# Optimization experiments

Measured on AMD Instinct MI355X. Metric: run time of the kernel, lower is better.

Reference implementation:

```python
import jax, jax.numpy as jnp
import numpy as np
import math

B, S, SIG, EMB, LAT, H, L_ENC, L_DEC = 16, 1024, 256, 256, 256, 8, 2, 2
EH, DH = EMB // H, LAT // H
EPS = 1e-10


def _sinusoidal_last_row(d):
    # last row of a standard sinusoidal PE table (position index = max_len-1)
    pos = 5000.0 - 1.0
    i = np.arange(d)
    angles = pos / np.power(10000.0, (2 * (i // 2)) / d)
    pe = np.where(i % 2 == 0, np.sin(angles), np.cos(angles))
    return jnp.asarray(pe, dtype=jnp.float32)


def setup_inputs() -> dict:
    key = jax.random.key(0)
    ks = iter(jax.random.split(key, 64))
    w = lambda *sh: 0.05 * jax.random.normal(next(ks), sh, dtype=jnp.float32)
    z = lambda *sh: jnp.zeros(sh, dtype=jnp.float32)
    d = {
        'inputData': jax.random.normal(next(ks), (B, S, SIG), dtype=jnp.float32),
        'pos_enc': _sinusoidal_last_row(SIG),
        'embW': w(SIG, EMB), 'embb': z(EMB),
        'qW': w(EMB, EMB), 'qb': z(EMB),
        'kW': w(EMB, EMB), 'kb': z(EMB),
        'vW': w(EMB, EMB), 'vb': z(EMB),
        'encBW': w(EH, EH), 'encBb': z(EH),
        'oW': w(EMB, EMB), 'ob': z(EMB),
        'ffe_W1': w(EMB, 2 * EMB), 'ffe_b1': z(2 * EMB),
        'ffe_W2': w(2 * EMB, EMB), 'ffe_b2': z(EMB),
        'lnSA_g': jnp.ones((L_ENC, EMB)), 'lnSA_b': z(L_ENC, EMB),
        'lnFF_g': jnp.ones((L_ENC, EMB)), 'lnFF_b': z(L_ENC, EMB),
        'start': w(1, LAT),
        'decQW': w(LAT, LAT), 'decQb': z(LAT),
        'decKW': w(EMB, EMB), 'decKb': z(EMB),
        'decVW': w(EMB, LAT), 'decVb': z(LAT),
        'decBW': w(EH + DH, DH), 'decBb': z(DH),
        'latW': w(LAT, LAT), 'latb': z(LAT),
        'ffd_W1': w(LAT, LAT // 2), 'ffd_b1': z(LAT // 2),
        'ffd_W2': w(LAT // 2, LAT), 'ffd_b2': z(LAT),
        'lnCA_g': jnp.ones((L_DEC, LAT)), 'lnCA_b': z(L_DEC, LAT),
        'lnLFF_g': jnp.ones((L_DEC, LAT)), 'lnLFF_b': z(L_DEC, LAT),
        'finW': w(LAT, LAT), 'finb': z(LAT),
    }
    return d


def _ln(x, g, b):
    m = x.mean(-1, keepdims=True)
    v = x.var(-1, keepdims=True)
    return (x - m) * jax.lax.rsqrt(v + EPS) * g + b


def _enc_attn(x, qW, qb, kW, kb, vW, vb, bW, bb, oW, ob):
    # x: (B,S,EMB) -> heads (B,H,S,EH)
    sp = lambda t: t.reshape(B, S, H, EH).transpose(0, 2, 1, 3)
    q, k, v = sp(x @ qW + qb), sp(x @ kW + kb), sp(x @ vW + vb)
    bk = k @ bW + bb                                   # bilinear key (B,H,S,EH)
    attn = jax.nn.softmax(jnp.einsum('bhqd,bhkd->bhqk', q, bk) / math.sqrt(EH), axis=-1)
    out = jnp.einsum('bhqk,bhkd->bhqd', attn, v)
    out = out.transpose(0, 2, 1, 3).reshape(B, S, EMB)
    return out @ oW + ob


def _dec_attn(enc, lat, qW, qb, kW, kb, vW, vb, bW, bb, oW, ob):
    # lat: (B,LAT) single query token; enc: (B,S,EMB)
    q = (lat @ qW + qb).reshape(B, 1, H, DH).transpose(0, 2, 1, 3)   # (B,H,1,DH)
    k = (enc @ kW + kb).reshape(B, S, H, EH).transpose(0, 2, 1, 3)   # (B,H,S,EH)
    v = (enc @ vW + vb).reshape(B, S, H, DH).transpose(0, 2, 1, 3)   # (B,H,S,DH)
    qcat = jnp.broadcast_to(q, (B, H, S, DH))
    kcat = jnp.concatenate([k, qcat], axis=-1)                       # (B,H,S,EH+DH)
    bk = kcat @ bW + bb                                              # (B,H,S,DH)
    attn = jax.nn.softmax(jnp.einsum('bhqd,bhkd->bhqk', q, bk) / math.sqrt(EH + DH), axis=-1)
    out = jnp.einsum('bhqk,bhkd->bhqd', attn, v)                     # (B,H,1,DH)
    out = out.transpose(0, 2, 1, 3).reshape(B, LAT)
    return out @ oW + ob


def reference(inputData, pos_enc, embW, embb, qW, qb, kW, kb, vW, vb, encBW, encBb,
              oW, ob, ffe_W1, ffe_b1, ffe_W2, ffe_b2, lnSA_g, lnSA_b, lnFF_g, lnFF_b,
              start, decQW, decQb, decKW, decKb, decVW, decVb, decBW, decBb,
              latW, latb, ffd_W1, ffd_b1, ffd_W2, ffd_b2, lnCA_g, lnCA_b,
              lnLFF_g, lnLFF_b, finW, finb):
    emb = (inputData + pos_enc) @ embW + embb          # (B,S,EMB)
    t = emb
    for l in range(L_ENC):
        n = _ln(t, lnSA_g[l], lnSA_b[l])
        a = _enc_attn(n, qW, qb, kW, kb, vW, vb, encBW, encBb, oW, ob) + n
        t = a + emb
        n2 = _ln(t, lnFF_g[l], lnFF_b[l])
        ff = jax.nn.selu(n2 @ ffe_W1 + ffe_b1) @ ffe_W2 + ffe_b2
        t = ff + n2
    init_lat = jnp.broadcast_to(start, (B, LAT))
    lat = init_lat
    for l in range(L_DEC):
        nl = _ln(init_lat, lnCA_g[l], lnCA_b[l])       # module always feeds initialLatentData
        lat = _dec_attn(t, nl, decQW, decQb, decKW, decKb, decVW, decVb,
                        decBW, decBb, latW, latb)
        nf = _ln(lat, lnLFF_g[l], lnLFF_b[l])
        lat = jax.nn.selu(nf @ ffd_W1 + ffd_b1) @ ffd_W2 + ffd_b2
    return lat @ finW + finb
```

## Files before the change

### kernel.cpp

```cpp
#include <hip/hip_runtime.h>
#include <hip/hip_bf16.h>
#include <math.h>

typedef __hip_bfloat16 bf16;

#define BB 16
#define SS 1024
#define NH 8
#define NR (BB*SS)
#define SZE ((size_t)NR*256)
#define RS 264
#define HS 520

typedef __attribute__((ext_vector_type(8))) short short8;
typedef __attribute__((ext_vector_type(4))) float f32x4;
typedef __attribute__((ext_vector_type(8))) unsigned short u16x8;
typedef __attribute__((ext_vector_type(4))) unsigned short u16x4;

__device__ __forceinline__ float bf2f(bf16 x){ return __bfloat162float(x); }
__device__ __forceinline__ bf16  f2bf(float x){ return __float2bfloat16(x); }
__device__ __forceinline__ unsigned short f2bfu(float x){
  bf16 t = __float2bfloat16(x); return *reinterpret_cast<unsigned short*>(&t);
}
__device__ __forceinline__ float bfu2f(unsigned short u){
  return __uint_as_float(((unsigned)u)<<16);
}

__device__ __forceinline__ float ldT(const float* p, size_t i){ return p[i]; }
__device__ __forceinline__ float ldT(const bf16*  p, size_t i){ return bf2f(p[i]); }
__device__ __forceinline__ void  stT(float* p, size_t i, float v){ p[i] = v; }
__device__ __forceinline__ void  stT(bf16*  p, size_t i, float v){ p[i] = f2bf(v); }

__device__ __forceinline__ float selu_f(float x){
  const float a = 1.6732632423543772f, sc = 1.0507009873554805f;
  return sc * (x > 0.f ? x : a * expm1f(x));
}

struct PtrPack { const void* p[43]; };
struct TabPack { int off[43]; int cnt[43]; int total; };
struct TrTab   { int srcOff[12]; int K[12]; int N[12]; int dstOff[12]; int total; };

__global__ __launch_bounds__(256) void k_canon(PtrPack ptrs, TabPack tab,
    float* __restrict__ dst, int* __restrict__ flagw)
{
  unsigned w0 = ((const unsigned*)ptrs.p[18])[0];
  int isbf = (w0 == 0x3F803F80u) ? 1 : 0;
  if (blockIdx.x == 0 && threadIdx.x == 0) *flagw = isbf;
  __shared__ int so[43], sn[43];
  int tid = threadIdx.x;
  if (tid < 43){ so[tid] = tab.off[tid]; sn[tid] = tab.cnt[tid]; }
  __syncthreads();
  int g = blockIdx.x*256 + tid;
  if (g >= tab.total) return;
  int seg = 1;
  while (seg < 42 && g >= so[seg] + sn[seg]) seg++;
  int li = g - so[seg];
  float v = isbf ? bf2f(((const bf16*)ptrs.p[seg])[li])
                 : ((const float*)ptrs.p[seg])[li];
  dst[g] = v;
}

__global__ __launch_bounds__(256) void k_transW(const float* __restrict__ wt,
    TrTab tt, unsigned short* __restrict__ dst)
{
  int g = blockIdx.x*256 + threadIdx.x;
  if (g >= tt.total) return;
  int seg = 0;
  while (seg < 11 && g >= tt.dstOff[seg] + tt.K[seg]*tt.N[seg]) seg++;
  int li = g - tt.dstOff[seg];
  int K = tt.K[seg], N = tt.N[seg];
  int n = li / K, k = li - n*K;
  dst[g] = f2bfu(wt[tt.srcOff[seg] + (size_t)k*N + n]);
}

template<int K, int LDA>
__device__ __forceinline__ void wave_gemm64(const unsigned short (*As)[LDA],
    const unsigned short* __restrict__ Wt, int n0, f32x4 acc[4][4], int lane)
{
  int col = lane & 15, quad = lane >> 4;
  #pragma unroll
  for (int k0 = 0; k0 < K; k0 += 32){
    short8 a[4], b[4];
    #pragma unroll
    for (int rt = 0; rt < 4; rt++)
      a[rt] = *(const short8*)(&As[rt*16 + col][k0 + quad*8]);
    #pragma unroll
    for (int ct = 0; ct < 4; ct++)
      b[ct] = *(const short8*)(&Wt[(size_t)(n0 + ct*16 + col)*K + k0 + quad*8]);
    #pragma unroll
    for (int rt = 0; rt < 4; rt++)
      #pragma unroll
      for (int ct = 0; ct < 4; ct++)
        acc[rt][ct] = __builtin_amdgcn_mfma_f32_16x16x32_bf16(a[rt], b[ct], acc[rt][ct], 0, 0, 0);
  }
}

#define ZERO_ACC(acc) { _Pragma("unroll") for (int rt=0;rt<4;rt++){ _Pragma("unroll") for (int ct=0;ct<4;ct++) acc[rt][ct] = (f32x4){0.f,0.f,0.f,0.f}; } }

#define EPI_BEGIN(e) { int rt = (e)>>4, ct = ((e)>>2)&3, r = (e)&3; \
    int lrow = rt*16 + quad*4 + r; int gcol0 = ct*16 + col; \
    float av = acc[rt][ct][r]; (void)lrow; (void)gcol0; (void)av;
#define EPI_END }

template<int PRE, typename OT>
__global__ __launch_bounds__(256) void k_gemm_mfma(const void* __restrict__ A,
    const int* __restrict__ flagp, const float* __restrict__ pe,
    const unsigned short* __restrict__ Wt, const float* __restrict__ bias,
    OT* __restrict__ out)
{
  __shared__ __align__(16) unsigned short As[64][RS];
  int tid = threadIdx.x, row0 = blockIdx.x*64;
  if (PRE == 0){
    int f = *flagp;
    for (int jj = 0; jj < 64; jj++){
      int idx = tid + jj*256, row = idx>>8, c = idx&255;
      size_t g = (size_t)(row0+row)*256 + c;
      float x = f ? bf2f(((const bf16*)A)[g]) : ((const float*)A)[g];
      As[row][c] = f2bfu(x + pe[c]);
    }
  } else {
    for (int jj = 0; jj < 64; jj++){
      int idx = tid + jj*256, row = idx>>8, c = idx&255;
      As[row][c] = f2bfu(((const float*)A)[(size_t)(row0+row)*256 + c]);
    }
  }
  __syncthreads();
  int w = tid>>6, lane = tid&63, col = lane&15, quad = lane>>4;
  f32x4 acc[4][4];
  ZERO_ACC(acc);
  wave_gemm64<256, RS>(As, Wt, w*64, acc, lane);
  #pragma unroll
  for (int e = 0; e < 64; e++){
    EPI_BEGIN(e)
    int grow = row0 + lrow, gcol = w*64 + gcol0;
    stT(out, (size_t)grow*256 + gcol, av + bias[gcol]);
    EPI_END
  }
}

__global__ __launch_bounds__(256) void k_qkvbk_mfma(const float* __restrict__ tsrc,
    const float* __restrict__ lng, const float* __restrict__ lnb,
    const unsigned short* __restrict__ qWt, const float* __restrict__ qb,
    const unsigned short* __restrict__ kWt, const float* __restrict__ kb,
    const unsigned short* __restrict__ vWt, const float* __restrict__ vb,
    const unsigned short* __restrict__ encBWt, const float* __restrict__ Bb,
    bf16* __restrict__ qo, bf16* __restrict__ vo, bf16* __restrict__ bko)
{
  __shared__ __align__(16) unsigned short Ns[64][RS];
  __shared__ __align__(16) unsigned short Ks[64][RS];
  __shared__ float mArr[64], rArr[64];
  int tid = threadIdx.x, row0 = blockIdx.x*64;
  int b = row0 >> 10, s0 = row0 & 1023;
  {
    int row = tid>>2, l4 = tid&3;
    const float* rp = tsrc + (size_t)(row0+row)*256;
    float s = 0.f, s2 = 0.f;
    for (int c = l4; c < 256; c += 4){ float x = rp[c]; s += x; s2 += x*x; }
    s  += __shfl_down(s, 2, 4);  s  += __shfl_down(s, 1, 4);
    s2 += __shfl_down(s2, 2, 4); s2 += __shfl_down(s2, 1, 4);
    if (l4 == 0){
      float m = s*(1.f/256.f);
      float v = s2*(1.f/256.f) - m*m;
      mArr[row] = m; rArr[row] = rsqrtf(fmaxf(v,0.f) + 1e-10f);
    }
  }
  __syncthreads();
  for (int jj = 0; jj < 64; jj++){
    int idx = tid + jj*256, row = idx>>8, c = idx&255;
    float x = tsrc[(size_t)(row0+row)*256 + c];
    Ns[row][c] = f2bfu((x - mArr[row])*rArr[row]*lng[c] + lnb[c]);
  }
  __syncthreads();
  int w = tid>>6, lane = tid&63, col = lane&15, quad = lane>>4;
  f32x4 acc[4][4];
  ZERO_ACC(acc);
  wave_gemm64<256, RS>(Ns, qWt, w*64, acc, lane);
  #pragma unroll
  for (int e = 0; e < 64; e++){
    EPI_BEGIN(e)
    int grow = row0 + lrow, gcol = w*64 + gcol0;
    qo[(size_t)grow*256 + gcol] = f2bf(av + qb[gcol]);
    EPI_END
  }
  ZERO_ACC(acc);
  wave_gemm64<256, RS>(Ns, vWt, w*64, acc, lane);
  #pragma unroll
  for (int e = 0; e < 64; e++){
    EPI_BEGIN(e)
    int grow = row0 + lrow, gcol = w*64 + gcol0;
    vo[(size_t)grow*256 + gcol] = f2bf(av + vb[gcol]);
    EPI_END
  }
  ZERO_ACC(acc);
  wave_gemm64<256, RS>(Ns, kWt, w*64, acc, lane);
  #pragma unroll
  for (int e = 0; e < 64; e++){
    EPI_BEGIN(e)
    int gcol = w*64 + gcol0;
    Ks[lrow][gcol] = f2bfu(av + kb[gcol]);
    EPI_END
  }
  __syncthreads();
  ZERO_ACC(acc);
  #pragma unroll
  for (int ct = 0; ct < 4; ct++){
    int base = w*64 + ct*16;
    int h = base >> 5, d0 = base & 31;
    short8 bfrag = *(const short8*)(&encBWt[(size_t)(d0 + col)*32 + quad*8]);
    #pragma unroll
    for (int rt = 0; rt < 4; rt++){
      short8 afrag = *(const short8*)(&Ks[rt*16 + col][h*32 + quad*8]);
      acc[rt][ct] = __builtin_amdgcn_mfma_f32_16x16x32_bf16(afrag, bfrag, acc[rt][ct], 0, 0, 0);
    }
  }
  #pragma unroll
  for (int e = 0; e < 64; e++){
    EPI_BEGIN(e)
    int srow = s0 + lrow;
    int gcol = w*64 + gcol0;
    int h = gcol >> 5, d = gcol & 31;
    bko[(((size_t)(b*NH+h))*SS + srow)*32 + d] = f2bf(av + Bb[d]);
    EPI_END
  }
}

__global__ __launch_bounds__(256) void k_attn_mfma(
    const bf16* __restrict__ q, const bf16* __restrict__ bk,
    const bf16* __restrict__ v, bf16* __restrict__ ao)
{
  int bi = blockIdx.x;
  int qt = bi & 15, h = (bi>>4)&7, b = bi>>7;
  int q0 = qt*64;
  int tid = threadIdx.x;
  int w = tid>>6, lane = tid&63;
  int quad = lane>>4, col = lane&15;

  __shared__ __align__(16) unsigned short Ks[64][32];
  __shared__ __align__(16) unsigned short Vt[32][72];
  __shared__ __align__(16) unsigned short Ps[4][16][72];

  const float scale = 0.17677669529663687f;
  short8 aq;
  {
    const unsigned short* gq = (const unsigned short*)q
        + ((size_t)(b*SS + q0 + w*16 + col))*256 + h*32 + quad*8;
    u16x8 qv = *(const u16x8*)gq;
    #pragma unroll
    for (int i=0;i<8;i++) aq[i] = (short)f2bfu(bfu2f(qv[i])*scale);
  }

  float l_r[4] = {0.f,0.f,0.f,0.f};
  f32x4 o0 = {0.f,0.f,0.f,0.f}, o1 = {0.f,0.f,0.f,0.f};

  for (int kt = 0; kt < 16; kt++){
    __syncthreads();
    {
      const u16x8* src = (const u16x8*)((const unsigned short*)bk
          + (((size_t)(b*NH+h))*SS + (size_t)kt*64)*32);
      ((u16x8*)&Ks[0][0])[tid] = src[tid];
    }
    #pragma unroll
    for (int it = 0; it < 2; it++){
      int idx = tid + it*256;
      int k = idx>>3, dg = idx&7;
      const unsigned short* gv = (const unsigned short*)v
          + ((size_t)(b*SS + kt*64 + k))*256 + h*32 + dg*4;
      u16x4 val = *(const u16x4*)gv;
      #pragma unroll
      for (int i=0;i<4;i++) Vt[dg*4+i][k] = val[i];
    }
    __syncthreads();
    f32x4 s[4];
    #pragma unroll
    for (int t4 = 0; t4 < 4; t4++){
      short8 bk8 = *(const short8*)(&Ks[t4*16 + col][quad*8]);
      s[t4] = __builtin_amdgcn_mfma_f32_16x16x32_bf16(aq, bk8,
                (f32x4){0.f,0.f,0.f,0.f}, 0, 0, 0);
    }
    #pragma unroll
    for (int r=0;r<4;r++){
      #pragma unroll
      for (int t4=0;t4<4;t4++){
        float p = __expf(s[t4][r]);
        l_r[r] += p;
        Ps[w][quad*4+r][t4*16+col] = f2bfu(p);
      }
    }
    __syncthreads();
    #pragma unroll
    for (int kk=0; kk<2; kk++){
      short8 ap  = *(const short8*)(&Ps[w][col][kk*32 + quad*8]);
      short8 bv0 = *(const short8*)(&Vt[col][kk*32 + quad*8]);
      short8 bv1 = *(const short8*)(&Vt[16+col][kk*32 + quad*8]);
      o0 = __builtin_amdgcn_mfma_f32_16x16x32_bf16(ap, bv0, o0, 0, 0, 0);
      o1 = __builtin_amdgcn_mfma_f32_16x16x32_bf16(ap, bv1, o1, 0, 0, 0);
    }
  }
  #pragma unroll
  for (int r=0;r<4;r++){
    #pragma unroll
    for (int msk=1; msk<16; msk<<=1) l_r[r] += __shfl_xor(l_r[r], msk, 64);
  }
  #pragma unroll
  for (int r=0;r<4;r++){
    float inv = 1.f / l_r[r];
    int qrow = q0 + w*16 + quad*4 + r;
    size_t o = ((size_t)(b*SS + qrow))*256 + h*32;
    ao[o + col]      = f2bf(o0[r]*inv);
    ao[o + 16 + col] = f2bf(o1[r]*inv);
  }
}

__global__ __launch_bounds__(256) void k_oproj_ffn_mfma(
    const float* __restrict__ tsrc, const float* __restrict__ emb,
    const bf16* __restrict__ ao,
    const float* __restrict__ lnSAg, const float* __restrict__ lnSAb,
    const unsigned short* __restrict__ oWt, const float* __restrict__ ob,
    const float* __restrict__ lnFFg, const float* __restrict__ lnFFb,
    const unsigned short* __restrict__ W1t, const float* __restrict__ b1,
    const unsigned short* __restrict__ W2t, const float* __restrict__ b2,
    float* __restrict__ tout)
{
  __shared__ __align__(16) unsigned short Ns[64][RS];
  __shared__ __align__(16) unsigned short Aos[64][RS];
  __shared__ __align__(16) unsigned short H1s[64][HS];
  __shared__ float mArr[64], rArr[64];
  int tid = threadIdx.x, row0 = blockIdx.x*64;
  {
    int row = tid>>2, l4 = tid&3;
    const float* rp = tsrc + (size_t)(row0+row)*256;
    float s = 0.f, s2 = 0.f;
    for (int c = l4; c < 256; c += 4){ float x = rp[c]; s += x; s2 += x*x; }
    s  += __shfl_down(s, 2, 4);  s  += __shfl_down(s, 1, 4);
    s2 += __shfl_down(s2, 2, 4); s2 += __shfl_down(s2, 1, 4);
    if (l4 == 0){
      float m = s*(1.f/256.f);
      float v = s2*(1.f/256.f) - m*m;
      mArr[row] = m; rArr[row] = rsqrtf(fmaxf(v,0.f) + 1e-10f);
    }
  }
  for (int jj = 0; jj < 64; jj++){
    int idx = tid + jj*256, row = idx>>8, c = idx&255;
    Aos[row][c] = ((const unsigned short*)ao)[(size_t)(row0+row)*256 + c];
  }
  __syncthreads();
  for (int jj = 0; jj < 64; jj++){
    int idx = tid + jj*256, row = idx>>8, c = idx&255;
    float x = tsrc[(size_t)(row0+row)*256 + c];
    Ns[row][c] = f2bfu((x - mArr[row])*rArr[row]*lnSAg[c] + lnSAb[c]);
  }
  __syncthreads();
  int w = tid>>6, lane = tid&63, col = lane&15, quad = lane>>4;
  f32x4 acc[4][4];
  ZERO_ACC(acc);
  wave_gemm64<256, RS>(Aos, oWt, w*64, acc, lane);
  __syncthreads();
  #pragma unroll
  for (int e = 0; e < 64; e++){
    EPI_BEGIN(e)
    int gcol = w*64 + gcol0;
    float tm = av + ob[gcol] + bfu2f(Ns[lrow][gcol])
             + emb[(size_t)(row0+lrow)*256 + gcol];
    Aos[lrow][gcol] = f2bfu(tm);
    EPI_END
  }
  __syncthreads();
  {
    int row = tid>>2, l4 = tid&3;
    float s = 0.f, s2 = 0.f;
    for (int c = l4; c < 256; c += 4){ float x = bfu2f(Aos[row][c]); s += x; s2 += x*x; }
    s  += __shfl_down(s, 2, 4);  s  += __shfl_down(s, 1, 4);
    s2 += __shfl_down(s2, 2, 4); s2 += __shfl_down(s2, 1, 4);
    if (l4 == 0){
      float m = s*(1.f/256.f);
      float v = s2*(1.f/256.f) - m*m;
      mArr[row] = m; rArr[row] = rsqrtf(fmaxf(v,0.f) + 1e-10f);
    }
  }
  __syncthreads();
  for (int jj = 0; jj < 64; jj++){
    int idx = tid + jj*256, row = idx>>8, c = idx&255;
    float x = bfu2f(Aos[row][c]);
    Ns[row][c] = f2bfu((x - mArr[row])*rArr[row]*lnFFg[c] + lnFFb[c]);
  }
  __syncthreads();
  #pragma unroll
  for (int p = 0; p < 2; p++){
    ZERO_ACC(acc);
    wave_gemm64<256, RS>(Ns, W1t, p*256 + w*64, acc, lane);
    #pragma unroll
    for (int e = 0; e < 64; e++){
      EPI_BEGIN(e)
      int gcol = p*256 + w*64 + gcol0;
      H1s[lrow][gcol] = f2bfu(selu_f(av + b1[gcol]));
      EPI_END
    }
  }
  __syncthreads();
  ZERO_ACC(acc);
  wave_gemm64<512, HS>(H1s, W2t, w*64, acc, lane);
  #pragma unroll
  for (int e = 0; e < 64; e++){
    EPI_BEGIN(e)
    int gcol = w*64 + gcol0;
    tout[(size_t)(row0+lrow)*256 + gcol] = av + b2[gcol] + bfu2f(Ns[lrow][gcol]);
    EPI_END
  }
}

__global__ __launch_bounds__(256) void k_dec_head(const float* __restrict__ startp,
    const float* __restrict__ lng, const float* __restrict__ lnb,
    const float* __restrict__ decQW, const float* __restrict__ decQb,
    const float* __restrict__ decBW,
    float* __restrict__ s_q, float* __restrict__ s_qc)
{
  __shared__ float s1[256], s2[256], nl[256], qv[256];
  int t = threadIdx.x;
  float v = startp[t];
  s1[t]=v; s2[t]=v*v; __syncthreads();
  for (int s=128;s>0;s>>=1){
    if (t<s){ s1[t]+=s1[t+s]; s2[t]+=s2[t+s]; }
    __syncthreads();
  }
  float m = s1[0]*(1.f/256.f);
  float var = s2[0]*(1.f/256.f) - m*m;
  float r = rsqrtf(fmaxf(var,0.f) + 1e-10f);
  nl[t] = (v-m)*r*lng[t] + lnb[t];
  __syncthreads();
  float acc = decQb[t];
  for (int k=0;k<256;k++) acc += nl[k]*decQW[k*256+t];
  qv[t] = acc; s_q[t] = acc;
  __syncthreads();
  int h = t>>5, d = t&31;
  float a = 0.f;
  #pragma unroll 8
  for (int e=0;e<32;e++) a += qv[h*32+e]*decBW[(32+e)*32 + d];
  s_qc[t] = a;
}

__global__ __launch_bounds__(256) void k_bkdec_mfma(const bf16* __restrict__ kk,
    const float* __restrict__ qc, const unsigned short* __restrict__ decBWt,
    const float* __restrict__ Bb, bf16* __restrict__ bko)
{
  __shared__ __align__(16) unsigned short Ks[64][RS];
  int tid = threadIdx.x, row0 = blockIdx.x*64;
  int b = row0 >> 10, s0 = row0 & 1023;
  for (int jj = 0; jj < 8; jj++){
    int idx = tid + jj*256;
    int row = idx>>5, c8 = idx&31;
    *(u16x8*)(&Ks[row][c8*8]) =
        *(const u16x8*)((const unsigned short*)kk + (size_t)(row0+row)*256 + c8*8);
  }
  __syncthreads();
  int w = tid>>6, lane = tid&63, col = lane&15, quad = lane>>4;
  f32x4 acc[4][4];
  ZERO_ACC(acc);
  #pragma unroll
  for (int ct = 0; ct < 4; ct++){
    int base = w*64 + ct*16;
    int h = base >> 5, d0 = base & 31;
    short8 bfrag = *(const short8*)(&decBWt[(size_t)(d0 + col)*32 + quad*8]);
    #pragma unroll
    for (int rt = 0; rt < 4; rt++){
      short8 afrag = *(const short8*)(&Ks[rt*16 + col][h*32 + quad*8]);
      acc[rt][ct] = __builtin_amdgcn_mfma_f32_16x16x32_bf16(afrag, bfrag, acc[rt][ct], 0, 0, 0);
    }
  }
  #pragma unroll
  for (int e = 0; e < 64; e++){
    EPI_BEGIN(e)
    int srow = s0 + lrow;
    int gcol = w*64 + gcol0;
    int h = gcol >> 5, d = gcol & 31;
    bko[(((size_t)(b*NH+h))*SS + srow)*32 + d] = f2bf(av + qc[gcol] + Bb[d]);
    EPI_END
  }
}

__global__ __launch_bounds__(256) void k_attn_dec(const float* __restrict__ q,
    const bf16* __restrict__ bk, const bf16* __restrict__ v,
    float* __restrict__ out)
{
  int h = blockIdx.x & 7, b = blockIdx.x >> 3;
  int tid = threadIdx.x;
  __shared__ float qs[32];
  __shared__ float sc[SS];
  __shared__ float red[256];
  if (tid < 32) qs[tid] = q[h*32 + tid] * 0.125f;
  __syncthreads();
  float lsum = 0.f;
  for (int jj=0;jj<4;jj++){
    int j = tid*4 + jj;
    size_t base = (((size_t)(b*NH+h))*SS + j)*32;
    float s = 0.f;
    #pragma unroll
    for (int d=0;d<32;d++) s += qs[d]*bf2f(bk[base + d]);
    float e = __expf(s);
    sc[j] = e; lsum += e;
  }
  red[tid] = lsum; __syncthreads();
  for (int s=128;s>0;s>>=1){ if (tid<s) red[tid]+=red[tid+s]; __syncthreads(); }
  float gs = red[0];
  __syncthreads();
  int d = tid & 31, c = tid >> 5;
  float acc = 0.f;
  for (int j=c*128; j<c*128+128; j++)
    acc += sc[j]*bf2f(v[((size_t)(b*SS + j))*256 + h*32 + d]);
  red[c*32+d] = acc;
  __syncthreads();
  if (tid < 32){
    float s = 0.f;
    #pragma unroll
    for (int cc=0;cc<8;cc++) s += red[cc*32+tid];
    out[b*256 + h*32 + tid] = s / gs;
  }
}

__global__ __launch_bounds__(256) void k_dec_tail(const float* __restrict__ s_ao,
    const float* __restrict__ latW, const float* __restrict__ latb,
    const float* __restrict__ lng, const float* __restrict__ lnb,
    const float* __restrict__ W1, const float* __restrict__ b1,
    const float* __restrict__ W2, const float* __restrict__ b2,
    const float* __restrict__ finW, const float* __restrict__ finb,
    const int* __restrict__ flagp, void* __restrict__ outv)
{
  __shared__ float x[256], y[256], s1[256], s2[256];
  int t = threadIdx.x, b = blockIdx.x;
  x[t] = s_ao[b*256 + t];
  __syncthreads();
  float lat = latb[t];
  for (int k=0;k<256;k++) lat += x[k]*latW[k*256+t];
  s1[t]=lat; s2[t]=lat*lat; __syncthreads();
  for (int s=128;s>0;s>>=1){
    if (t<s){ s1[t]+=s1[t+s]; s2[t]+=s2[t+s]; }
    __syncthreads();
  }
  float m = s1[0]*(1.f/256.f);
  float var = s2[0]*(1.f/256.f) - m*m;
  float r = rsqrtf(fmaxf(var,0.f) + 1e-10f);
  y[t] = (lat-m)*r*lng[t] + lnb[t];
  __syncthreads();
  if (t < 128){
    float a2 = b1[t];
    for (int k=0;k<256;k++) a2 += y[k]*W1[k*128+t];
    x[t] = selu_f(a2);
  }
  __syncthreads();
  float a3 = b2[t];
  for (int k=0;k<128;k++) a3 += x[k]*W2[k*256+t];
  s1[t] = a3;
  __syncthreads();
  float o = finb[t];
  for (int k=0;k<256;k++) o += s1[k]*finW[k*256+t];
  size_t oi = (size_t)b*256 + t;
  if (*flagp) ((bf16*)outv)[oi] = f2bf(o);
  else        ((float*)outv)[oi] = o;
}

extern "C" void kernel_launch(void* const* d_in, const int* in_sizes, int n_in,
                              void* d_out, int out_size, void* d_ws, size_t ws_size,
                              hipStream_t stream)
{
  static const int cnts[43] = {
    0,256,65536,256,65536,256,65536,256,65536,256,1024,32,65536,256,
    131072,512,131072,256,512,512,512,512,256,65536,256,65536,256,65536,256,
    2048,32,65536,256,32768,128,32768,256,512,512,512,512,65536,256 };
  TabPack tab; int acc0 = 0;
  for (int i = 0; i < 43; i++){ tab.off[i] = acc0; tab.cnt[i] = cnts[i]; acc0 += cnts[i]; }
  tab.total = acc0;
  PtrPack ptrs;
  for (int i = 0; i < 43; i++) ptrs.p[i] = d_in[i];

  char* p = (char*)d_ws;
  float* wt   = (float*)p;
  int*  flagp = (int*)(p + (4u<<20));
  char* bigc  = p + (4u<<20) + 256;
  float* g_emb = (float*)bigc;
  float* g_t   = (float*)(bigc + SZE*4);
  bf16*  g_q   = (bf16*)(bigc + 2*SZE*4);
  bf16*  g_v   = (bf16*)(bigc + 2*SZE*4 + SZE*2);
  bf16*  g_ao  = (bf16*)(bigc + 2*SZE*4 + 2*SZE*2);
  bf16*  g_bk  = (bf16*)(bigc + 2*SZE*4 + 3*SZE*2);
  float* fsm   = (float*)(bigc + 2*SZE*4 + 4*SZE*2);
  unsigned short* wtr = (unsigned short*)(bigc + 2*SZE*4 + 4*SZE*2 + 131072*4);
  float* s_q  = fsm;
  float* s_qc = fsm + 256;
  float* s_ao = fsm + 512;

  static const int trIdx[10] = {2,4,6,8,12,14,16,25,27,10};
  static const int trK[10]   = {256,256,256,256,256,256,512,256,256,32};
  static const int trN[10]   = {256,256,256,256,256,512,256,256,256,32};
  TrTab tr; int tacc = 0;
  for (int i = 0; i < 10; i++){
    tr.srcOff[i] = tab.off[trIdx[i]];
    tr.K[i] = trK[i]; tr.N[i] = trN[i];
    tr.dstOff[i] = tacc; tacc += trK[i]*trN[i];
  }
  tr.srcOff[10] = tab.off[29];        tr.K[10]=32; tr.N[10]=32; tr.dstOff[10]=tacc; tacc+=1024;
  tr.srcOff[11] = tab.off[29] + 1024; tr.K[11]=32; tr.N[11]=32; tr.dstOff[11]=tacc; tacc+=1024;
  tr.total = tacc;
  const unsigned short *embWt = wtr + tr.dstOff[0], *qWt = wtr + tr.dstOff[1],
    *kWt = wtr + tr.dstOff[2], *vWt = wtr + tr.dstOff[3], *oWt = wtr + tr.dstOff[4],
    *ffeW1t = wtr + tr.dstOff[5], *ffeW2t = wtr + tr.dstOff[6],
    *decKWt = wtr + tr.dstOff[7], *decVWt = wtr + tr.dstOff[8],
    *encBWt = wtr + tr.dstOff[9], *decBWtk = wtr + tr.dstOff[10];

  #define WP(i) (wt + tab.off[i])
  const float *pe=WP(1), *embb=WP(3), *qb=WP(5), *kb=WP(7), *vb=WP(9),
    *encBb=WP(11), *ob=WP(13), *ffeb1=WP(15), *ffeb2=WP(17),
    *lnSAg=WP(18), *lnSAb=WP(19), *lnFFg=WP(20), *lnFFb=WP(21),
    *startp=WP(22), *decQW=WP(23), *decQb=WP(24), *decKb=WP(26),
    *decVb=WP(28), *decBW=WP(29), *decBb=WP(30), *latW=WP(31),
    *latb=WP(32), *ffdW1=WP(33), *ffdb1=WP(34), *ffdW2=WP(35), *ffdb2=WP(36),
    *lnCAg=WP(37), *lnCAb=WP(38), *lnLFFg=WP(39), *lnLFFb=WP(40),
    *finW=WP(41), *finb=WP(42);

  dim3 blk(256);
  const int G64 = NR/64;
  const int GM  = BB*NH*(SS/64);
  const int LD  = 1;

  k_canon<<<(tab.total+255)/256, blk, 0, stream>>>(ptrs, tab, wt, flagp);
  k_transW<<<(tr.total+255)/256, blk, 0, stream>>>(wt, tr, wtr);

  k_gemm_mfma<0,float><<<G64, blk, 0, stream>>>(d_in[0], flagp, pe, embWt, embb, g_emb);

  const float* tcur = g_emb;
  for (int l = 0; l < 2; l++){
    k_qkvbk_mfma<<<G64, blk, 0, stream>>>(tcur, lnSAg+l*256, lnSAb+l*256,
        qWt, qb, kWt, kb, vWt, vb, encBWt, encBb, g_q, g_v, g_bk);
    k_attn_mfma<<<GM, blk, 0, stream>>>(g_q, g_bk, g_v, g_ao);
    k_oproj_ffn_mfma<<<G64, blk, 0, stream>>>(tcur, g_emb, g_ao,
        lnSAg+l*256, lnSAb+l*256, oWt, ob, lnFFg+l*256, lnFFb+l*256,
        ffeW1t, ffeb1, ffeW2t, ffeb2, g_t);
    tcur = g_t;
  }

  k_dec_head<<<1, blk, 0, stream>>>(startp, lnCAg+LD*256, lnCAb+LD*256,
      decQW, decQb, decBW, s_q, s_qc);
  k_gemm_mfma<1,bf16><<<G64, blk, 0, stream>>>(g_t, flagp, pe, decKWt, decKb, g_q);
  k_gemm_mfma<1,bf16><<<G64, blk, 0, stream>>>(g_t, flagp, pe, decVWt, decVb, g_v);
  k_bkdec_mfma<<<G64, blk, 0, stream>>>(g_q, s_qc, decBWtk, decBb, g_bk);
  k_attn_dec<<<BB*NH, blk, 0, stream>>>(s_q, g_bk, g_v, s_ao);
  k_dec_tail<<<BB, blk, 0, stream>>>(s_ao, latW, latb, lnLFFg+LD*256, lnLFFb+LD*256,
      ffdW1, ffdb1, ffdW2, ffdb2, finW, finb, flagp, d_out);
  #undef WP
}
```

Measured before the change: 565.9 us.

## Split GEMM kernels over N halves and retile encoder attention with double buffering

```diff
diff --git a/kernel.cpp b/kernel.cpp
--- a/kernel.cpp
+++ b/kernel.cpp
@@ -11,6 +11,7 @@
 #define SZE ((size_t)NR*256)
 #define RS 264
 #define HS 520
+#define KS2 136
 
 typedef __attribute__((ext_vector_type(8))) short short8;
 typedef __attribute__((ext_vector_type(4))) float f32x4;
@@ -73,29 +74,30 @@
   dst[g] = f2bfu(wt[tt.srcOff[seg] + (size_t)k*N + n]);
 }
 
-template<int K, int LDA>
-__device__ __forceinline__ void wave_gemm64(const unsigned short (*As)[LDA],
-    const unsigned short* __restrict__ Wt, int n0, f32x4 acc[4][4], int lane)
+template<int K, int LDA, int CT>
+__device__ __forceinline__ void wave_gemmN(const unsigned short (*As)[LDA],
+    const unsigned short* __restrict__ Wt, int n0, f32x4 acc[4][CT], int lane)
 {
   int col = lane & 15, quad = lane >> 4;
   #pragma unroll
   for (int k0 = 0; k0 < K; k0 += 32){
-    short8 a[4], b[4];
+    short8 a[4], b[CT];
     #pragma unroll
     for (int rt = 0; rt < 4; rt++)
       a[rt] = *(const short8*)(&As[rt*16 + col][k0 + quad*8]);
     #pragma unroll
-    for (int ct = 0; ct < 4; ct++)
+    for (int ct = 0; ct < CT; ct++)
       b[ct] = *(const short8*)(&Wt[(size_t)(n0 + ct*16 + col)*K + k0 + quad*8]);
     #pragma unroll
     for (int rt = 0; rt < 4; rt++)
       #pragma unroll
-      for (int ct = 0; ct < 4; ct++)
+      for (int ct = 0; ct < CT; ct++)
         acc[rt][ct] = __builtin_amdgcn_mfma_f32_16x16x32_bf16(a[rt], b[ct], acc[rt][ct], 0, 0, 0);
   }
 }
 
-#define ZERO_ACC(acc) { _Pragma("unroll") for (int rt=0;rt<4;rt++){ _Pragma("unroll") for (int ct=0;ct<4;ct++) acc[rt][ct] = (f32x4){0.f,0.f,0.f,0.f}; } }
+#define ZERO_ACC4(acc) { _Pragma("unroll") for (int rt=0;rt<4;rt++){ _Pragma("unroll") for (int ct=0;ct<4;ct++) acc[rt][ct] = (f32x4){0.f,0.f,0.f,0.f}; } }
+#define ZERO_ACC2(acc) { _Pragma("unroll") for (int rt=0;rt<4;rt++){ _Pragma("unroll") for (int ct=0;ct<2;ct++) acc[rt][ct] = (f32x4){0.f,0.f,0.f,0.f}; } }
 
 #define EPI_BEGIN(e) { int rt = (e)>>4, ct = ((e)>>2)&3, r = (e)&3; \
     int lrow = rt*16 + quad*4 + r; int gcol0 = ct*16 + col; \
@@ -109,7 +111,9 @@
     OT* __restrict__ out)
 {
   __shared__ __align__(16) unsigned short As[64][RS];
-  int tid = threadIdx.x, row0 = blockIdx.x*64;
+  int tid = threadIdx.x;
+  int m = blockIdx.x & 255, nh = blockIdx.x >> 8;
+  int row0 = m*64;
   if (PRE == 0){
     int f = *flagp;
     for (int jj = 0; jj < 64; jj++){
@@ -126,15 +130,21 @@
   }
   __syncthreads();
   int w = tid>>6, lane = tid&63, col = lane&15, quad = lane>>4;
-  f32x4 acc[4][4];
-  ZERO_ACC(acc);
-  wave_gemm64<256, RS>(As, Wt, w*64, acc, lane);
-  #pragma unroll
-  for (int e = 0; e < 64; e++){
-    EPI_BEGIN(e)
-    int grow = row0 + lrow, gcol = w*64 + gcol0;
-    stT(out, (size_t)grow*256 + gcol, av + bias[gcol]);
-    EPI_END
+  int n0 = nh*128 + w*32;
+  f32x4 acc[4][2];
+  ZERO_ACC2(acc);
+  wave_gemmN<256, RS, 2>(As, Wt, n0, acc, lane);
+  #pragma unroll
+  for (int rt = 0; rt < 4; rt++){
+    #pragma unroll
+    for (int ct = 0; ct < 2; ct++){
+      #pragma unroll
+      for (int r = 0; r < 4; r++){
+        int grow = row0 + rt*16 + quad*4 + r;
+        int gcol = n0 + ct*16 + col;
+        stT(out, (size_t)grow*256 + gcol, acc[rt][ct][r] + bias[gcol]);
+      }
+    }
   }
 }
 
@@ -147,9 +157,11 @@
     bf16* __restrict__ qo, bf16* __restrict__ vo, bf16* __restrict__ bko)
 {
   __shared__ __align__(16) unsigned short Ns[64][RS];
-  __shared__ __align__(16) unsigned short Ks[64][RS];
+  __shared__ __align__(16) unsigned short Ks[64][KS2];
   __shared__ float mArr[64], rArr[64];
-  int tid = threadIdx.x, row0 = blockIdx.x*64;
+  int tid = threadIdx.x;
+  int m = blockIdx.x & 255, nh = blockIdx.x >> 8;
+  int row0 = m*64;
   int b = row0 >> 10, s0 = row0 & 1023;
   {
     int row = tid>>2, l4 = tid&3;
@@ -159,9 +171,9 @@
     s  += __shfl_down(s, 2, 4);  s  += __shfl_down(s, 1, 4);
     s2 += __shfl_down(s2, 2, 4); s2 += __shfl_down(s2, 1, 4);
     if (l4 == 0){
-      float m = s*(1.f/256.f);
-      float v = s2*(1.f/256.f) - m*m;
-      mArr[row] = m; rArr[row] = rsqrtf(fmaxf(v,0.f) + 1e-10f);
+      float mn = s*(1.f/256.f);
+      float v = s2*(1.f/256.f) - mn*mn;
+      mArr[row] = mn; rArr[row] = rsqrtf(fmaxf(v,0.f) + 1e-10f);
     }
   }
   __syncthreads();
@@ -172,55 +184,73 @@
   }
   __syncthreads();
   int w = tid>>6, lane = tid&63, col = lane&15, quad = lane>>4;
-  f32x4 acc[4][4];
-  ZERO_ACC(acc);
-  wave_gemm64<256, RS>(Ns, qWt, w*64, acc, lane);
-  #pragma unroll
-  for (int e = 0; e < 64; e++){
-    EPI_BEGIN(e)
-    int grow = row0 + lrow, gcol = w*64 + gcol0;
-    qo[(size_t)grow*256 + gcol] = f2bf(av + qb[gcol]);
-    EPI_END
-  }
-  ZERO_ACC(acc);
-  wave_gemm64<256, RS>(Ns, vWt, w*64, acc, lane);
-  #pragma unroll
-  for (int e = 0; e < 64; e++){
-    EPI_BEGIN(e)
-    int grow = row0 + lrow, gcol = w*64 + gcol0;
-    vo[(size_t)grow*256 + gcol] = f2bf(av + vb[gcol]);
-    EPI_END
-  }
-  ZERO_ACC(acc);
-  wave_gemm64<256, RS>(Ns, kWt, w*64, acc, lane);
-  #pragma unroll
-  for (int e = 0; e < 64; e++){
-    EPI_BEGIN(e)
-    int gcol = w*64 + gcol0;
-    Ks[lrow][gcol] = f2bfu(av + kb[gcol]);
-    EPI_END
-  }
-  __syncthreads();
-  ZERO_ACC(acc);
-  #pragma unroll
-  for (int ct = 0; ct < 4; ct++){
-    int base = w*64 + ct*16;
-    int h = base >> 5, d0 = base & 31;
-    short8 bfrag = *(const short8*)(&encBWt[(size_t)(d0 + col)*32 + quad*8]);
+  int n0 = nh*128 + w*32;
+  f32x4 acc[4][2];
+  ZERO_ACC2(acc);
+  wave_gemmN<256, RS, 2>(Ns, qWt, n0, acc, lane);
+  #pragma unroll
+  for (int rt = 0; rt < 4; rt++){
+    #pragma unroll
+    for (int ct = 0; ct < 2; ct++){
+      #pragma unroll
+      for (int r = 0; r < 4; r++){
+        int grow = row0 + rt*16 + quad*4 + r;
+        int gcol = n0 + ct*16 + col;
+        qo[(size_t)grow*256 + gcol] = f2bf(acc[rt][ct][r] + qb[gcol]);
+      }
+    }
+  }
+  ZERO_ACC2(acc);
+  wave_gemmN<256, RS, 2>(Ns, vWt, n0, acc, lane);
+  #pragma unroll
+  for (int rt = 0; rt < 4; rt++){
+    #pragma unroll
+    for (int ct = 0; ct < 2; ct++){
+      #pragma unroll
+      for (int r = 0; r < 4; r++){
+        int grow = row0 + rt*16 + quad*4 + r;
+        int gcol = n0 + ct*16 + col;
+        vo[(size_t)grow*256 + gcol] = f2bf(acc[rt][ct][r] + vb[gcol]);
+      }
+    }
+  }
+  ZERO_ACC2(acc);
+  wave_gemmN<256, RS, 2>(Ns, kWt, n0, acc, lane);
+  #pragma unroll
+  for (int rt = 0; rt < 4; rt++){
+    #pragma unroll
+    for (int ct = 0; ct < 2; ct++){
+      #pragma unroll
+      for (int r = 0; r < 4; r++){
+        int lrow = rt*16 + quad*4 + r;
+        int lcol = w*32 + ct*16 + col;
+        Ks[lrow][lcol] = f2bfu(acc[rt][ct][r] + kb[nh*128 + lcol]);
+      }
+    }
+  }
+  __syncthreads();
+  int h = nh*4 + w;
+  ZERO_ACC2(acc);
+  #pragma unroll
+  for (int ct = 0; ct < 2; ct++){
+    short8 bfrag = *(const short8*)(&encBWt[(size_t)(ct*16 + col)*32 + quad*8]);
     #pragma unroll
     for (int rt = 0; rt < 4; rt++){
-      short8 afrag = *(const short8*)(&Ks[rt*16 + col][h*32 + quad*8]);
+      short8 afrag = *(const short8*)(&Ks[rt*16 + col][w*32 + quad*8]);
       acc[rt][ct] = __builtin_amdgcn_mfma_f32_16x16x32_bf16(afrag, bfrag, acc[rt][ct], 0, 0, 0);
     }
   }
   #pragma unroll
-  for (int e = 0; e < 64; e++){
-    EPI_BEGIN(e)
-    int srow = s0 + lrow;
-    int gcol = w*64 + gcol0;
-    int h = gcol >> 5, d = gcol & 31;
-    bko[(((size_t)(b*NH+h))*SS + srow)*32 + d] = f2bf(av + Bb[d]);
-    EPI_END
+  for (int rt = 0; rt < 4; rt++){
+    #pragma unroll
+    for (int ct = 0; ct < 2; ct++){
+      #pragma unroll
+      for (int r = 0; r < 4; r++){
+        int srow = s0 + rt*16 + quad*4 + r;
+        int d = ct*16 + col;
+        bko[(((size_t)(b*NH+h))*SS + srow)*32 + d] = f2bf(acc[rt][ct][r] + Bb[d]);
+      }
+    }
   }
 }
 
@@ -229,35 +259,43 @@
     const bf16* __restrict__ v, bf16* __restrict__ ao)
 {
   int bi = blockIdx.x;
-  int qt = bi & 15, h = (bi>>4)&7, b = bi>>7;
-  int q0 = qt*64;
+  int qq = bi >> 7, b = (bi >> 3) & 15, h = bi & 7;
   int tid = threadIdx.x;
   int w = tid>>6, lane = tid&63;
   int quad = lane>>4, col = lane&15;
-
-  __shared__ __align__(16) unsigned short Ks[64][32];
-  __shared__ __align__(16) unsigned short Vt[32][72];
-  __shared__ __align__(16) unsigned short Ps[4][16][72];
+  int q0 = qq*256 + w*64;
+
+  __shared__ __align__(16) unsigned short Ks2b[2][64][32];
+  __shared__ __align__(16) unsigned short Vt2b[2][32][72];
+  __shared__ __align__(16) unsigned short Ps[4][64][72];
 
   const float scale = 0.17677669529663687f;
-  short8 aq;
-  {
+  short8 aq[4];
+  #pragma unroll
+  for (int rt = 0; rt < 4; rt++){
     const unsigned short* gq = (const unsigned short*)q
-        + ((size_t)(b*SS + q0 + w*16 + col))*256 + h*32 + quad*8;
+        + ((size_t)(b*SS + q0 + rt*16 + col))*256 + h*32 + quad*8;
     u16x8 qv = *(const u16x8*)gq;
     #pragma unroll
-    for (int i=0;i<8;i++) aq[i] = (short)f2bfu(bfu2f(qv[i])*scale);
-  }
-
-  float l_r[4] = {0.f,0.f,0.f,0.f};
-  f32x4 o0 = {0.f,0.f,0.f,0.f}, o1 = {0.f,0.f,0.f,0.f};
+    for (int i=0;i<8;i++) aq[rt][i] = (short)f2bfu(bfu2f(qv[i])*scale);
+  }
+
+  float l_r[4][4];
+  f32x4 o0[4], o1[4];
+  #pragma unroll
+  for (int rt=0;rt<4;rt++){
+    o0[rt] = (f32x4){0.f,0.f,0.f,0.f};
+    o1[rt] = (f32x4){0.f,0.f,0.f,0.f};
+    #pragma unroll
+    for (int r=0;r<4;r++) l_r[rt][r] = 0.f;
+  }
 
   for (int kt = 0; kt < 16; kt++){
-    __syncthreads();
+    int cb = kt & 1;
     {
       const u16x8* src = (const u16x8*)((const unsigned short*)bk
           + (((size_t)(b*NH+h))*SS + (size_t)kt*64)*32);
-      ((u16x8*)&Ks[0][0])[tid] = src[tid];
+      ((u16x8*)&Ks2b[cb][0][0])[tid] = src[tid];
     }
     #pragma unroll
     for (int it = 0; it < 2; it++){
@@ -267,47 +305,57 @@
           + ((size_t)(b*SS + kt*64 + k))*256 + h*32 + dg*4;
       u16x4 val = *(const u16x4*)gv;
       #pragma unroll
-      for (int i=0;i<4;i++) Vt[dg*4+i][k] = val[i];
+      for (int i=0;i<4;i++) Vt2b[cb][dg*4+i][k] = val[i];
     }
     __syncthreads();
-    f32x4 s[4];
-    #pragma unroll
-    for (int t4 = 0; t4 < 4; t4++){
-      short8 bk8 = *(const short8*)(&Ks[t4*16 + col][quad*8]);
-      s[t4] = __builtin_amdgcn_mfma_f32_16x16x32_bf16(aq, bk8,
-                (f32x4){0.f,0.f,0.f,0.f}, 0, 0, 0);
-    }
+    short8 bk8[4];
+    #pragma unroll
+    for (int t4 = 0; t4 < 4; t4++)
+      bk8[t4] = *(const short8*)(&Ks2b[cb][t4*16 + col][quad*8]);
+    #pragma unroll
+    for (int rt = 0; rt < 4; rt++){
+      f32x4 s[4];
+      #pragma unroll
+      for (int t4 = 0; t4 < 4; t4++)
+        s[t4] = __builtin_amdgcn_mfma_f32_16x16x32_bf16(aq[rt], bk8[t4],
+                  (f32x4){0.f,0.f,0.f,0.f}, 0, 0, 0);
+      #pragma unroll
+      for (int r=0;r<4;r++){
+        #pragma unroll
+        for (int t4=0;t4<4;t4++){
+          float pv = __expf(s[t4][r]);
+          l_r[rt][r] += pv;
+          Ps[w][rt*16 + quad*4 + r][t4*16 + col] = f2bfu(pv);
+        }
+      }
+    }
+    short8 bv00 = *(const short8*)(&Vt2b[cb][col][quad*8]);
+    short8 bv10 = *(const short8*)(&Vt2b[cb][col][32 + quad*8]);
+    short8 bv01 = *(const short8*)(&Vt2b[cb][16+col][quad*8]);
+    short8 bv11 = *(const short8*)(&Vt2b[cb][16+col][32 + quad*8]);
+    #pragma unroll
+    for (int rt = 0; rt < 4; rt++){
+      short8 ap0 = *(const short8*)(&Ps[w][rt*16 + col][quad*8]);
+      short8 ap1 = *(const short8*)(&Ps[w][rt*16 + col][32 + quad*8]);
+      o0[rt] = __builtin_amdgcn_mfma_f32_16x16x32_bf16(ap0, bv00, o0[rt], 0, 0, 0);
+      o0[rt] = __builtin_amdgcn_mfma_f32_16x16x32_bf16(ap1, bv10, o0[rt], 0, 0, 0);
+      o1[rt] = __builtin_amdgcn_mfma_f32_16x16x32_bf16(ap0, bv01, o1[rt], 0, 0, 0);
+      o1[rt] = __builtin_amdgcn_mfma_f32_16x16x32_bf16(ap1, bv11, o1[rt], 0, 0, 0);
+    }
+  }
+  #pragma unroll
+  for (int rt=0;rt<4;rt++){
     #pragma unroll
     for (int r=0;r<4;r++){
-      #pragma unroll
-      for (int t4=0;t4<4;t4++){
-        float p = __expf(s[t4][r]);
-        l_r[r] += p;
-        Ps[w][quad*4+r][t4*16+col] = f2bfu(p);
-      }
-    }
-    __syncthreads();
-    #pragma unroll
-    for (int kk=0; kk<2; kk++){
-      short8 ap  = *(const short8*)(&Ps[w][col][kk*32 + quad*8]);
-      short8 bv0 = *(const short8*)(&Vt[col][kk*32 + quad*8]);
-      short8 bv1 = *(const short8*)(&Vt[16+col][kk*32 + quad*8]);
-      o0 = __builtin_amdgcn_mfma_f32_16x16x32_bf16(ap, bv0, o0, 0, 0, 0);
-      o1 = __builtin_amdgcn_mfma_f32_16x16x32_bf16(ap, bv1, o1, 0, 0, 0);
-    }
-  }
-  #pragma unroll
-  for (int r=0;r<4;r++){
-    #pragma unroll
-    for (int msk=1; msk<16; msk<<=1) l_r[r] += __shfl_xor(l_r[r], msk, 64);
-  }
-  #pragma unroll
-  for (int r=0;r<4;r++){
-    float inv = 1.f / l_r[r];
-    int qrow = q0 + w*16 + quad*4 + r;
-    size_t o = ((size_t)(b*SS + qrow))*256 + h*32;
-    ao[o + col]      = f2bf(o0[r]*inv);
-    ao[o + 16 + col] = f2bf(o1[r]*inv);
+      float l = l_r[rt][r];
+      #pragma unroll
+      for (int msk=1; msk<16; msk<<=1) l += __shfl_xor(l, msk, 64);
+      float inv = 1.f / l;
+      int qrow = q0 + rt*16 + quad*4 + r;
+      size_t o = ((size_t)(b*SS + qrow))*256 + h*32;
+      ao[o + col]      = f2bf(o0[rt][r]*inv);
+      ao[o + 16 + col] = f2bf(o1[rt][r]*inv);
+    }
   }
 }
 
@@ -352,8 +400,8 @@
   __syncthreads();
   int w = tid>>6, lane = tid&63, col = lane&15, quad = lane>>4;
   f32x4 acc[4][4];
-  ZERO_ACC(acc);
-  wave_gemm64<256, RS>(Aos, oWt, w*64, acc, lane);
+  ZERO_ACC4(acc);
+  wave_gemmN<256, RS, 4>(Aos, oWt, w*64, acc, lane);
   __syncthreads();
   #pragma unroll
   for (int e = 0; e < 64; e++){
@@ -386,8 +434,8 @@
   __syncthreads();
   #pragma unroll
   for (int p = 0; p < 2; p++){
-    ZERO_ACC(acc);
-    wave_gemm64<256, RS>(Ns, W1t, p*256 + w*64, acc, lane);
+    ZERO_ACC4(acc);
+    wave_gemmN<256, RS, 4>(Ns, W1t, p*256 + w*64, acc, lane);
     #pragma unroll
     for (int e = 0; e < 64; e++){
       EPI_BEGIN(e)
@@ -397,8 +445,8 @@
     }
   }
   __syncthreads();
-  ZERO_ACC(acc);
-  wave_gemm64<512, HS>(H1s, W2t, w*64, acc, lane);
+  ZERO_ACC4(acc);
+  wave_gemmN<512, HS, 4>(H1s, W2t, w*64, acc, lane);
   #pragma unroll
   for (int e = 0; e < 64; e++){
     EPI_BEGIN(e)
@@ -454,7 +502,7 @@
   __syncthreads();
   int w = tid>>6, lane = tid&63, col = lane&15, quad = lane>>4;
   f32x4 acc[4][4];
-  ZERO_ACC(acc);
+  ZERO_ACC4(acc);
   #pragma unroll
   for (int ct = 0; ct < 4; ct++){
     int base = w*64 + ct*16;
@@ -616,20 +664,21 @@
     *finW=WP(41), *finb=WP(42);
 
   dim3 blk(256);
-  const int G64 = NR/64;
-  const int GM  = BB*NH*(SS/64);
-  const int LD  = 1;
+  const int G64  = NR/64;
+  const int GSP  = 512;
+  const int GA2  = 512;
+  const int LD   = 1;
 
   k_canon<<<(tab.total+255)/256, blk, 0, stream>>>(ptrs, tab, wt, flagp);
   k_transW<<<(tr.total+255)/256, blk, 0, stream>>>(wt, tr, wtr);
 
-  k_gemm_mfma<0,float><<<G64, blk, 0, stream>>>(d_in[0], flagp, pe, embWt, embb, g_emb);
+  k_gemm_mfma<0,float><<<GSP, blk, 0, stream>>>(d_in[0], flagp, pe, embWt, embb, g_emb);
 
   const float* tcur = g_emb;
   for (int l = 0; l < 2; l++){
-    k_qkvbk_mfma<<<G64, blk, 0, stream>>>(tcur, lnSAg+l*256, lnSAb+l*256,
+    k_qkvbk_mfma<<<GSP, blk, 0, stream>>>(tcur, lnSAg+l*256, lnSAb+l*256,
         qWt, qb, kWt, kb, vWt, vb, encBWt, encBb, g_q, g_v, g_bk);
-    k_attn_mfma<<<GM, blk, 0, stream>>>(g_q, g_bk, g_v, g_ao);
+    k_attn_mfma<<<GA2, blk, 0, stream>>>(g_q, g_bk, g_v, g_ao);
     k_oproj_ffn_mfma<<<G64, blk, 0, stream>>>(tcur, g_emb, g_ao,
         lnSAg+l*256, lnSAb+l*256, oWt, ob, lnFFg+l*256, lnFFb+l*256,
         ffeW1t, ffeb1, ffeW2t, ffeb2, g_t);
@@ -638,8 +687,8 @@
 
   k_dec_head<<<1, blk, 0, stream>>>(startp, lnCAg+LD*256, lnCAb+LD*256,
       decQW, decQb, decBW, s_q, s_qc);
-  k_gemm_mfma<1,bf16><<<G64, blk, 0, stream>>>(g_t, flagp, pe, decKWt, decKb, g_q);
-  k_gemm_mfma<1,bf16><<<G64, blk, 0, stream>>>(g_t, flagp, pe, decVWt, decVb, g_v);
+  k_gemm_mfma<1,bf16><<<GSP, blk, 0, stream>>>(g_t, flagp, pe, decKWt, decKb, g_q);
+  k_gemm_mfma<1,bf16><<<GSP, blk, 0, stream>>>(g_t, flagp, pe, decVWt, decVb, g_v);
   k_bkdec_mfma<<<G64, blk, 0, stream>>>(g_q, s_qc, decBWtk, decBb, g_bk);
   k_attn_dec<<<BB*NH, blk, 0, stream>>>(s_q, g_bk, g_v, s_ao);
   k_dec_tail<<<BB, blk, 0, stream>>>(s_ao, latW, latb, lnLFFg+LD*256, lnLFFb+LD*256,
```

Result: slower. 642.2 us (+13.5%).
